# Kernel tuning notes

Measured on AMD Instinct MI355X. Metric: run time of the kernel, lower is better.

Reference implementation:

```python
import jax, jax.numpy as jnp
import numpy as np

EPS = 1e-5  # BatchNorm eps


def _unfold3x3(x):
    """torch.nn.Unfold(kernel=3, pad=1, stride=1) -> [B, H*W, 9, C] layout.

    Kernel positions are row-major (kh, kw); index 4 is the center, matching
    x_pn[:, :, 4:5, :] in the torch module.
    """
    B, C, H, W = x.shape
    xp = jnp.pad(x, ((0, 0), (0, 0), (1, 1), (1, 1)))
    patches = jnp.stack([xp[:, :, i:i + H, j:j + W]
                         for i in range(3) for j in range(3)], axis=1)  # [B,9,C,H,W]
    return patches.transpose(0, 3, 4, 1, 2).reshape(B, H * W, 9, C)


def setup_inputs() -> dict:
    key = jax.random.key(0)
    ks = jax.random.split(key, 10)
    B, Cin, Cout, H, W = 2, 64, 64, 64, 2048
    Ctot = 4 + Cin  # 4 meta channels + feature channels
    return {
        "x": jax.random.normal(ks[0], (B, Ctot, H, W), jnp.float32),
        "mask": jax.random.randint(ks[1], (B, 1, H, W), 0, 2, jnp.int32),
        # weight_mlp1: Linear(4 -> Cin, bias=False), torch layout [out, in]
        "W1": jax.random.normal(ks[2], (Cin, 4), jnp.float32) * 0.3,
        "bn1_g": jnp.ones((Cin,), jnp.float32),
        "bn1_b": jnp.zeros((Cin,), jnp.float32),
        "bn1_m": jax.random.normal(ks[3], (Cin,), jnp.float32) * 0.1,
        "bn1_v": jax.random.uniform(ks[4], (Cin,), jnp.float32, 0.5, 1.5),
        # weight_mlp2: Linear(Cin -> 1) (attention head)
        "W2": jax.random.normal(ks[5], (1, Cin), jnp.float32) * 0.1,
        "b2": jnp.zeros((1,), jnp.float32),
        # aggregation_mlp: Linear(9*Cin -> Cout, bias=False)
        "Wagg": jax.random.normal(ks[6], (Cout, 9 * Cin), jnp.float32) * 0.04,
        "bn2_g": jnp.ones((Cout,), jnp.float32),
        "bn2_b": jnp.zeros((Cout,), jnp.float32),
        "bn2_m": jax.random.normal(ks[7], (Cout,), jnp.float32) * 0.1,
        "bn2_v": jax.random.uniform(ks[8], (Cout,), jnp.float32, 0.5, 1.5),
    }


def reference(x, mask, W1, bn1_g, bn1_b, bn1_m, bn1_v, W2, b2,
              Wagg, bn2_g, bn2_b, bn2_m, bn2_v):
    B, Ctot, H, W_ = x.shape
    Cin = W1.shape[0]

    xu = _unfold3x3(x)                       # [B, HW, 9, Ctot]
    feats = xu[..., 4:]                      # [B, HW, 9, Cin]
    pn = xu[..., :4]                         # meta coords of 9 neighbors
    d = pn - pn[:, :, 4:5, :]                # relative to center pixel

    # per-neighbor weight MLP (Linear -> BN(eval) -> ReLU -> Linear)
    w = jnp.einsum('bnkm,cm->bnkc', d, W1)   # [B, HW, 9, Cin]
    w = (w - bn1_m) * (bn1_g * jax.lax.rsqrt(bn1_v + EPS)) + bn1_b
    w = jax.nn.relu(w)
    w = jnp.einsum('bnkc,oc->bnko', w, W2) + b2  # [B, HW, 9, 1]

    mu = _unfold3x3(mask.astype(jnp.float32))    # [B, HW, 9, 1]
    w = w * mu                                   # masked logits
    w = jax.nn.softmax(w[..., 0], axis=-1)[..., None]  # attention over 9 neighbors

    out = (w * feats).reshape(B, H * W_, 9 * Cin)
    y = jnp.einsum('bnf,of->bno', out, Wagg)     # [B, HW, Cout]
    y = (y - bn2_m) * (bn2_g * jax.lax.rsqrt(bn2_v + EPS)) + bn2_b
    y = jax.nn.relu(y)
    # Fold(kernel=1) == reshape back to the feature map
    return y.transpose(0, 2, 1).reshape(B, -1, H, W_)
```

## Files before the change

kernel.cpp:

```cpp
#include <hip/hip_runtime.h>
#include <hip/hip_bf16.h>

#define H_ 64
#define W_ 2048
#define HWsz (H_*W_)
#define CIN 64
#define CTOT 68
#define COUT 64

typedef float  f32x2  __attribute__((ext_vector_type(2)));
typedef float  f32x4  __attribute__((ext_vector_type(4)));
typedef float  f32x16 __attribute__((ext_vector_type(16)));
typedef short  s16x8  __attribute__((ext_vector_type(8)));

__device__ __forceinline__ unsigned short f2bf(float f) {
    unsigned u = __builtin_bit_cast(unsigned, f);
    unsigned r = u + 0x7fffu + ((u >> 16) & 1u);
    return (unsigned short)(r >> 16);
}

__device__ __forceinline__ unsigned pack2bf(float a, float b) {
    __hip_bfloat162 h = __float22bfloat162_rn(float2{a, b});
    unsigned u;
    __builtin_memcpy(&u, &h, 4);
    return u;
}

__device__ __forceinline__ void gl_lds16(const unsigned short* g, unsigned short* l) {
    __builtin_amdgcn_global_load_lds(
        (const __attribute__((address_space(1))) unsigned int*)g,
        (__attribute__((address_space(3))) unsigned int*)l,
        16, 0, 0);
}

__global__ __launch_bounds__(256) void prep_bw(
    const float* __restrict__ Wagg,
    const float* __restrict__ W1, const float* __restrict__ g1,
    const float* __restrict__ b1, const float* __restrict__ m1,
    const float* __restrict__ v1, const float* __restrict__ W2,
    unsigned short* __restrict__ BwS, float* __restrict__ Wfold)
{
    int tid = threadIdx.x;
    if (blockIdx.x == 0) {
        if (tid < 64) {
            float s1 = g1[tid] * rsqrtf(v1[tid] + 1e-5f);
#pragma unroll
            for (int m = 0; m < 4; ++m) Wfold[tid*8 + m] = W1[tid*4 + m] * s1;
            Wfold[tid*8 + 4] = b1[tid] - m1[tid]*s1;
            Wfold[tid*8 + 5] = W2[tid];
            Wfold[tid*8 + 6] = 0.f;
            Wfold[tid*8 + 7] = 0.f;
        }
        __syncthreads();
        if (tid == 0) {
            float s = 0.f;
            for (int c = 0; c < 64; ++c) s += fmaxf(Wfold[c*8 + 4], 0.f) * Wfold[c*8 + 5];
            Wfold[512] = s;
        }
    }
    int idx = blockIdx.x * 256 + tid;
    if (idx < 4608) {
        int lane = idx & 63;
        int rest = idx >> 6;
        int nt = rest & 1;
        int ks = (rest >> 1) & 3;
        int k9 = rest >> 3;
        int o  = nt*32 + (lane & 31);
        int ch = ks*16 + (lane >> 5)*8;
        const float* src = Wagg + (size_t)o*(9*CIN) + k9*64 + ch;
        s16x8 v8;
#pragma unroll
        for (int j = 0; j < 8; ++j) v8[j] = (short)f2bf(src[j]);
        *(s16x8*)(BwS + (size_t)idx*8) = v8;
    }
}

__global__ __launch_bounds__(512, 6) void sw_k(
    const float* __restrict__ x, const int* __restrict__ mask,
    const float* __restrict__ Wfold, const float* __restrict__ b2p,
    float* __restrict__ sws, unsigned short* __restrict__ xg)
{
    __shared__ float sw[2][9][64];

    const int tid = threadIdx.x;
    const int bx = blockIdx.x, by = blockIdx.y;
    const int b = by >> 5, h0 = (by & 31) << 1;
    const int w0 = bx << 6;
    const int lane = tid & 63, wv = tid >> 6;

    const float* xp = x + (size_t)b*CTOT*HWsz;
    const float* xf = x + ((size_t)b*CTOT + 4)*HWsz;
    const int*   mk = mask + (size_t)b*HWsz;

    float tv[2][8];
#pragma unroll
    for (int cc = 0; cc < 2; ++cc) {
        int id = tid + (cc << 9);
        int rq = id >> 9, g = (id >> 6) & 7, pxx = id & 63;
        const float* src = xf + (size_t)(g*8)*HWsz + (size_t)(h0 + rq)*W_ + w0 + pxx;
#pragma unroll
        for (int j = 0; j < 8; ++j) tv[cc][j] = src[(size_t)j*HWsz];
    }

    const int px = lane, gw = w0 + px;
    const int rowq = wv >> 2, tg = wv & 3;
    const int h = h0 + rowq;
    const int ka = 2*tg + (tg >> 1);

    float pc[4];
#pragma unroll
    for (int ch = 0; ch < 4; ++ch) pc[ch] = xp[(size_t)ch*HWsz + (size_t)h*W_ + gw];

    f32x2 dd[4]; f32x2 mu;
#pragma unroll
    for (int i = 0; i < 2; ++i) {
        int k = ka + i;
        int r = k/3 - 1, d = k%3 - 1;
        int ih = h + r, iw = gw + d;
        bool ok = ((unsigned)ih < (unsigned)H_) && ((unsigned)iw < (unsigned)W_);
        int ihc = min(max(ih, 0), H_-1);
        int iwc = min(max(iw, 0), W_-1);
        mu[i] = ok ? (float)mk[(size_t)ihc*W_ + iwc] : 0.f;
#pragma unroll
        for (int ch = 0; ch < 4; ++ch) {
            float p = xp[(size_t)ch*HWsz + (size_t)ihc*W_ + iwc];
            dd[ch][i] = (ok ? p : 0.f) - pc[ch];
        }
    }

    const f32x4* Wf4 = (const f32x4*)Wfold;
    const f32x2 z2 = {0.f, 0.f};
    f32x2 lg = z2;
#pragma unroll 8
    for (int c = 0; c < CIN; ++c) {
        f32x4 wa = Wf4[2*c];
        f32x4 wb = Wf4[2*c + 1];
        f32x2 v = {wb[0], wb[0]};
        v = dd[0]*wa[0] + v;
        v = dd[1]*wa[1] + v;
        v = dd[2]*wa[2] + v;
        v = dd[3]*wa[3] + v;
        v = __builtin_elementwise_max(v, z2);
        lg = v*wb[1] + lg;
    }
    float b2v = b2p[0];
    sw[rowq][ka    ][px] = (lg[0] + b2v) * mu[0];
    sw[rowq][ka + 1][px] = (lg[1] + b2v) * mu[1];

#pragma unroll
    for (int cc = 0; cc < 2; ++cc) {
        int id = tid + (cc << 9);
        int rq = id >> 9, g = (id >> 6) & 7, pxx = id & 63;
        uint4 q;
        q.x = pack2bf(tv[cc][0], tv[cc][1]); q.y = pack2bf(tv[cc][2], tv[cc][3]);
        q.z = pack2bf(tv[cc][4], tv[cc][5]); q.w = pack2bf(tv[cc][6], tv[cc][7]);
        *(uint4*)(xg + ((((size_t)(b*H_ + h0 + rq)*8 + g)*W_) + w0 + pxx)*8) = q;
    }
    __syncthreads();

    if (tid < 128) {
        int rq = tid >> 6, p2 = tid & 63;
        float mu4 = (float)mk[(size_t)(h0 + rq)*W_ + w0 + p2];
        float lgv[9];
#pragma unroll
        for (int k = 0; k < 9; ++k) if (k != 4) lgv[k] = sw[rq][k][p2];
        lgv[4] = (Wfold[512] + b2v) * mu4;
        float mx = -1e30f;
#pragma unroll
        for (int k = 0; k < 9; ++k) mx = fmaxf(mx, lgv[k]);
        float s = 0.f, e[9];
#pragma unroll
        for (int k = 0; k < 9; ++k) { e[k] = __expf(lgv[k] - mx); s += e[k]; }
        float inv = 1.f / s;
        float* dst = sws + ((size_t)(b*H_ + h0 + rq)*9)*W_ + w0 + p2;
#pragma unroll
        for (int k = 0; k < 9; ++k) dst[(size_t)k*W_] = e[k] * inv;
    }
}

__global__ __launch_bounds__(256, 4) void agg_k(
    const unsigned short* __restrict__ xg, const float* __restrict__ sws,
    const unsigned short* __restrict__ BwS,
    const float* __restrict__ g2, const float* __restrict__ bb2,
    const float* __restrict__ m2, const float* __restrict__ v2,
    float* __restrict__ out)
{
    __shared__ __align__(16) unsigned short fe[4][8][66][8];
    __shared__ __align__(16) float sbn[2][64];

    const int tid = threadIdx.x;
    const int bx = blockIdx.x, by = blockIdx.y;
    const int b = by >> 5, h0 = (by & 31) << 1;
    const int w0 = bx << 6;
    const int lane = tid & 63, wv = tid >> 6;

#pragma unroll
    for (int it = 0; it < 8; ++it) {
        int u = it*4 + wv;
        int g = u & 7, r = u >> 3;
        int gr = h0 - 1 + r;
        if ((unsigned)gr < (unsigned)H_) {
            const unsigned short* src =
                xg + ((((size_t)(b*H_ + gr)*8 + g)*W_) + w0 + lane)*8;
            gl_lds16(src, &fe[r][g][1][0]);
        } else {
            uint4 z = {0u, 0u, 0u, 0u};
            *(uint4*)&fe[r][g][1 + lane][0] = z;
        }
    }
    if (tid < 64) {
        int c2 = tid & 1, g = (tid >> 1) & 7, r = tid >> 4;
        int gr = h0 - 1 + r, gc = w0 - 1 + c2*65;
        uint4 q = {0u, 0u, 0u, 0u};
        if (((unsigned)gr < (unsigned)H_) && ((unsigned)gc < (unsigned)W_))
            q = *(const uint4*)(xg + ((((size_t)(b*H_ + gr)*8 + g)*W_) + gc)*8);
        *(uint4*)&fe[r][g][c2*65][0] = q;
    }
    if (tid >= 64 && tid < 128) {
        int o = tid - 64;
        float sc = g2[o] * rsqrtf(v2[o] + 1e-5f);
        sbn[0][o] = sc;
        sbn[1][o] = bb2[o] - m2[o]*sc;
    }

    const int nt = wv & 1, rh = wv >> 1;
    const int l31 = lane & 31, l5 = lane >> 5;
    const int hC = h0 + rh;
    const float* swp = sws + ((size_t)(b*H_ + hC)*9)*W_ + w0 + l31;
    float swr[2][9];
#pragma unroll
    for (int half = 0; half < 2; ++half)
#pragma unroll
        for (int k9 = 0; k9 < 9; ++k9)
            swr[half][k9] = swp[(size_t)k9*W_ + half*32];

    __syncthreads();

    const f32x16 fz16 = {0.f,0.f,0.f,0.f,0.f,0.f,0.f,0.f,0.f,0.f,0.f,0.f,0.f,0.f,0.f,0.f};
    f32x16 fin[2] = {fz16, fz16};

#pragma unroll
    for (int k9 = 0; k9 < 9; ++k9) {
        const int rr = rh + k9/3;
        const int dwp = k9 % 3;

        s16x8 aw[4];
#pragma unroll
        for (int ks = 0; ks < 4; ++ks)
            aw[ks] = *(const s16x8*)(BwS + (size_t)((((k9<<2) + ks)*2 + nt) << 9) + lane*8);

#pragma unroll
        for (int half = 0; half < 2; ++half) {
            int col = half*32 + l31 + dwp;
            f32x16 tmp = fz16;
#pragma unroll
            for (int ks = 0; ks < 4; ++ks) {
                s16x8 bfr = *(const s16x8*)&fe[rr][ks*2 + l5][col][0];
                tmp = __builtin_amdgcn_mfma_f32_32x32x16_bf16(aw[ks], bfr, tmp, 0, 0, 0);
            }
            float wsc = swr[half][k9];
#pragma unroll
            for (int c = 0; c < 16; ++c) fin[half][c] += wsc * tmp[c];
        }
    }

    int obase = nt*32 + 4*l5;
#pragma unroll
    for (int half = 0; half < 2; ++half) {
        float* od = out + (((size_t)b*COUT + obase)*H_ + hC)*W_ + w0 + half*32 + l31;
#pragma unroll
        for (int v = 0; v < 4; ++v) {
            f32x4 sc4 = *(const f32x4*)&sbn[0][obase + 8*v];
            f32x4 tc4 = *(const f32x4*)&sbn[1][obase + 8*v];
#pragma unroll
            for (int c = 0; c < 4; ++c)
                od[(size_t)(8*v + c)*HWsz] =
                    fmaxf(fmaf(fin[half][4*v + c], sc4[c], tc4[c]), 0.f);
        }
    }
}

extern "C" void kernel_launch(void* const* d_in, const int* in_sizes, int n_in,
                              void* d_out, int out_size, void* d_ws, size_t ws_size,
                              hipStream_t stream)
{
    const float* x    = (const float*)d_in[0];
    const int*   mask = (const int*)d_in[1];
    const float* W1   = (const float*)d_in[2];
    const float* g1   = (const float*)d_in[3];
    const float* b1   = (const float*)d_in[4];
    const float* m1   = (const float*)d_in[5];
    const float* v1   = (const float*)d_in[6];
    const float* W2   = (const float*)d_in[7];
    const float* b2   = (const float*)d_in[8];
    const float* Wagg = (const float*)d_in[9];
    const float* g2   = (const float*)d_in[10];
    const float* bb2  = (const float*)d_in[11];
    const float* m2   = (const float*)d_in[12];
    const float* v2   = (const float*)d_in[13];
    float* outp = (float*)d_out;

    char* ws = (char*)d_ws;
    unsigned short* BwS   = (unsigned short*)(ws + 0);
    float*          Wfold = (float*)(ws + 73728);
    float*          sws   = (float*)(ws + 76800);
    unsigned short* xg    = (unsigned short*)(ws + 9513984);

    hipLaunchKernelGGL(prep_bw, dim3(18), dim3(256), 0, stream,
                       Wagg, W1, g1, b1, m1, v1, W2, BwS, Wfold);
    hipLaunchKernelGGL(sw_k, dim3(W_/64, 64), dim3(512), 0, stream,
                       x, mask, Wfold, b2, sws, xg);
    hipLaunchKernelGGL(agg_k, dim3(W_/64, 64), dim3(256), 0, stream,
                       xg, sws, BwS, g2, bb2, m2, v2, outp);
}
```

Baseline: 188.9 us.

## Compute attention weight MLP with fp16 MFMA instead of scalar FMA loop

The per-neighbor weight MLP (4->64 linear with folded BN) in sw_k now runs as 32x32x16 fp16 MFMA tiles. Weights are pre-packed into an fp16 A-fragment and a W2 lookup table by prep_bw, and the neighbor deltas are packed as B-fragments with the bias carried through a constant-one lane. ReLU and the dot with W2 are applied on the accumulator registers and then reduced across half-waves. The feature-transpose loads are moved after this compute, which shortens their live range. The change lowers the VALU work but rounds the deltas and weights to fp16 and adds cross-lane shuffles.

```diff
diff --git a/kernel.cpp b/kernel.cpp
--- a/kernel.cpp
+++ b/kernel.cpp
@@ -12,6 +12,7 @@
 typedef float  f32x4  __attribute__((ext_vector_type(4)));
 typedef float  f32x16 __attribute__((ext_vector_type(16)));
 typedef short  s16x8  __attribute__((ext_vector_type(8)));
+typedef _Float16 f16x8 __attribute__((ext_vector_type(8)));
 
 __device__ __forceinline__ unsigned short f2bf(float f) {
     unsigned u = __builtin_bit_cast(unsigned, f);
@@ -38,7 +39,8 @@
     const float* __restrict__ W1, const float* __restrict__ g1,
     const float* __restrict__ b1, const float* __restrict__ m1,
     const float* __restrict__ v1, const float* __restrict__ W2,
-    unsigned short* __restrict__ BwS, float* __restrict__ Wfold)
+    unsigned short* __restrict__ BwS, float* __restrict__ Wfold,
+    unsigned short* __restrict__ AfS, float* __restrict__ w2tab)
 {
     int tid = threadIdx.x;
     if (blockIdx.x == 0) {
@@ -50,6 +52,30 @@
             Wfold[tid*8 + 5] = W2[tid];
             Wfold[tid*8 + 6] = 0.f;
             Wfold[tid*8 + 7] = 0.f;
+        }
+        if (tid >= 64 && tid < 192) {
+            int idx = tid - 64;
+            int mh = idx >> 6, l = idx & 63;
+            int ch = mh*32 + (l & 31);
+            int kb = (l >> 5) * 8;
+            float s1 = g1[ch] * rsqrtf(v1[ch] + 1e-5f);
+            unsigned short o8[8];
+#pragma unroll
+            for (int j = 0; j < 8; ++j) {
+                int k = kb + j;
+                float val = (k < 4) ? W1[ch*4 + k] * s1
+                          : (k == 4 ? b1[ch] - m1[ch]*s1 : 0.f);
+                _Float16 hv = (_Float16)val;
+                o8[j] = __builtin_bit_cast(unsigned short, hv);
+            }
+#pragma unroll
+            for (int j = 0; j < 8; ++j) AfS[(size_t)idx*8 + j] = o8[j];
+        }
+        if (tid >= 192) {
+            int t = tid - 192;
+            int mh = t >> 5, hi = (t >> 4) & 1, r = t & 15;
+            int ch = mh*32 + (r & 3) + 8*(r >> 2) + 4*hi;
+            w2tab[t] = W2[ch];
         }
         __syncthreads();
         if (tid == 0) {
@@ -78,6 +104,7 @@
 __global__ __launch_bounds__(512, 6) void sw_k(
     const float* __restrict__ x, const int* __restrict__ mask,
     const float* __restrict__ Wfold, const float* __restrict__ b2p,
+    const unsigned short* __restrict__ AfS, const float* __restrict__ w2tab,
     float* __restrict__ sws, unsigned short* __restrict__ xg)
 {
     __shared__ float sw[2][9][64];
@@ -92,20 +119,13 @@
     const float* xf = x + ((size_t)b*CTOT + 4)*HWsz;
     const int*   mk = mask + (size_t)b*HWsz;
 
-    float tv[2][8];
-#pragma unroll
-    for (int cc = 0; cc < 2; ++cc) {
-        int id = tid + (cc << 9);
-        int rq = id >> 9, g = (id >> 6) & 7, pxx = id & 63;
-        const float* src = xf + (size_t)(g*8)*HWsz + (size_t)(h0 + rq)*W_ + w0 + pxx;
-#pragma unroll
-        for (int j = 0; j < 8; ++j) tv[cc][j] = src[(size_t)j*HWsz];
-    }
-
     const int px = lane, gw = w0 + px;
     const int rowq = wv >> 2, tg = wv & 3;
     const int h = h0 + rowq;
     const int ka = 2*tg + (tg >> 1);
+
+    f16x8 Af0 = *(const f16x8*)(AfS + (size_t)lane*8);
+    f16x8 Af1 = *(const f16x8*)(AfS + 512 + (size_t)lane*8);
 
     float pc[4];
 #pragma unroll
@@ -128,25 +148,68 @@
         }
     }
 
-    const f32x4* Wf4 = (const f32x4*)Wfold;
-    const f32x2 z2 = {0.f, 0.f};
-    f32x2 lg = z2;
-#pragma unroll 8
-    for (int c = 0; c < CIN; ++c) {
-        f32x4 wa = Wf4[2*c];
-        f32x4 wb = Wf4[2*c + 1];
-        f32x2 v = {wb[0], wb[0]};
-        v = dd[0]*wa[0] + v;
-        v = dd[1]*wa[1] + v;
-        v = dd[2]*wa[2] + v;
-        v = dd[3]*wa[3] + v;
-        v = __builtin_elementwise_max(v, z2);
-        lg = v*wb[1] + lg;
+    float ddp[4][2], mup2[2];
+#pragma unroll
+    for (int j = 0; j < 4; ++j)
+#pragma unroll
+        for (int i = 0; i < 2; ++i) ddp[j][i] = __shfl_xor(dd[j][i], 32);
+    mup2[0] = __shfl_xor(mu[0], 32);
+    mup2[1] = __shfl_xor(mu[1], 32);
+
+    const bool lo = lane < 32;
+    const _Float16 hz = (_Float16)0.f;
+    const _Float16 h1 = lo ? (_Float16)1.f : hz;
+    f16x8 Bf[4];
+#pragma unroll
+    for (int i = 0; i < 2; ++i)
+#pragma unroll
+        for (int p = 0; p < 2; ++p) {
+            f16x8 f;
+#pragma unroll
+            for (int j = 0; j < 4; ++j) {
+                float v = p ? ddp[j][i] : dd[j][i];
+                f[j] = lo ? (_Float16)v : hz;
+            }
+            f[4] = h1; f[5] = hz; f[6] = hz; f[7] = hz;
+            Bf[i*2 + p] = f;
+        }
+
+    const int hi = lane >> 5;
+    const f32x16 fz16 = {0.f,0.f,0.f,0.f,0.f,0.f,0.f,0.f,0.f,0.f,0.f,0.f,0.f,0.f,0.f,0.f};
+    float acc[4] = {0.f, 0.f, 0.f, 0.f};
+#pragma unroll
+    for (int mh = 0; mh < 2; ++mh) {
+        const float* wp = w2tab + mh*32 + hi*16;
+        f32x4 wq[4];
+#pragma unroll
+        for (int q = 0; q < 4; ++q) wq[q] = *(const f32x4*)(wp + 4*q);
+        f16x8 A = mh ? Af1 : Af0;
+#pragma unroll
+        for (int tp = 0; tp < 4; ++tp) {
+            f32x16 C = __builtin_amdgcn_mfma_f32_32x32x16_f16(A, Bf[tp], fz16, 0, 0, 0);
+#pragma unroll
+            for (int r = 0; r < 16; ++r)
+                acc[tp] = fmaf(fmaxf(C[r], 0.f), wq[r >> 2][r & 3], acc[tp]);
+        }
     }
     float b2v = b2p[0];
-    sw[rowq][ka    ][px] = (lg[0] + b2v) * mu[0];
-    sw[rowq][ka + 1][px] = (lg[1] + b2v) * mu[1];
-
+#pragma unroll
+    for (int tp = 0; tp < 4; ++tp) {
+        float full = acc[tp] + __shfl_xor(acc[tp], 32);
+        int i = tp >> 1, p = tp & 1;
+        float lw = (full + b2v) * (p ? mup2[i] : mu[i]);
+        if (lo) sw[rowq][ka + i][p*32 + lane] = lw;
+    }
+
+    float tv[2][8];
+#pragma unroll
+    for (int cc = 0; cc < 2; ++cc) {
+        int id = tid + (cc << 9);
+        int rq = id >> 9, g = (id >> 6) & 7, pxx = id & 63;
+        const float* src = xf + (size_t)(g*8)*HWsz + (size_t)(h0 + rq)*W_ + w0 + pxx;
+#pragma unroll
+        for (int j = 0; j < 8; ++j) tv[cc][j] = src[(size_t)j*HWsz];
+    }
 #pragma unroll
     for (int cc = 0; cc < 2; ++cc) {
         int id = tid + (cc << 9);
@@ -303,13 +366,15 @@
     char* ws = (char*)d_ws;
     unsigned short* BwS   = (unsigned short*)(ws + 0);
     float*          Wfold = (float*)(ws + 73728);
-    float*          sws   = (float*)(ws + 76800);
-    unsigned short* xg    = (unsigned short*)(ws + 9513984);
+    unsigned short* AfS   = (unsigned short*)(ws + 76800);
+    float*          w2tab = (float*)(ws + 78848);
+    float*          sws   = (float*)(ws + 81920);
+    unsigned short* xg    = (unsigned short*)(ws + 9519104);
 
     hipLaunchKernelGGL(prep_bw, dim3(18), dim3(256), 0, stream,
-                       Wagg, W1, g1, b1, m1, v1, W2, BwS, Wfold);
+                       Wagg, W1, g1, b1, m1, v1, W2, BwS, Wfold, AfS, w2tab);
     hipLaunchKernelGGL(sw_k, dim3(W_/64, 64), dim3(512), 0, stream,
-                       x, mask, Wfold, b2, sws, xg);
+                       x, mask, Wfold, b2, AfS, w2tab, sws, xg);
     hipLaunchKernelGGL(agg_k, dim3(W_/64, 64), dim3(256), 0, stream,
                        xg, sws, BwS, g2, bb2, m2, v2, outp);
 }
```

Result: slower. 318.4 us (+68.5%).
